# Kernel optimization log

Measured on AMD Instinct MI355X. Metric: run time of the kernel, lower is better.

## Reference

```python
import jax, jax.numpy as jnp
import numpy as np

B, N, D = 8, 1024, 768
H = 12
HD = D // H


def setup_inputs() -> dict:
    key = jax.random.key(0)
    ks = jax.random.split(key, 9)
    s = 1.0 / np.sqrt(D)
    return {
        "x": jax.random.normal(ks[0], (B, N, D), dtype=jnp.float32),
        "Wq": jax.random.normal(ks[1], (D, D), dtype=jnp.float32) * s,
        "bq": jax.random.normal(ks[2], (D,), dtype=jnp.float32) * 0.02,
        "Wk": jax.random.normal(ks[3], (D, D), dtype=jnp.float32) * s,
        "bk": jax.random.normal(ks[4], (D,), dtype=jnp.float32) * 0.02,
        "Wv": jax.random.normal(ks[5], (D, D), dtype=jnp.float32) * s,
        "bv": jax.random.normal(ks[6], (D,), dtype=jnp.float32) * 0.02,
        "Wo": jax.random.normal(ks[7], (D, D), dtype=jnp.float32) * s,
        "bo": jax.random.normal(ks[8], (D,), dtype=jnp.float32) * 0.02,
    }


def _softmax_one(x):
    # quiet softmax: exp(x - max) / (1 + sum exp(x - max))
    x = x - jnp.max(x, axis=-1, keepdims=True)
    ex = jnp.exp(x)
    return ex / (1.0 + jnp.sum(ex, axis=-1, keepdims=True))


def reference(x, Wq, bq, Wk, bk, Wv, bv, Wo, bo):
    q = x @ Wq + bq  # [B,N,D]
    k = x @ Wk + bk
    v = x @ Wv + bv
    # split heads -> [B,H,N,HD]
    qs = q.reshape(B, N, H, HD).transpose(0, 2, 1, 3)
    ks = k.reshape(B, N, H, HD).transpose(0, 2, 1, 3)
    vs = v.reshape(B, N, H, HD).transpose(0, 2, 1, 3)
    scores = jnp.einsum("bhqd,bhkd->bhqk", qs, ks) / np.sqrt(HD)
    attn = _softmax_one(scores)  # quiet_attention=True
    ctx = jnp.einsum("bhqk,bhkd->bhqd", attn, vs)
    ctx = ctx.transpose(0, 2, 1, 3).reshape(B, N, D)
    return ctx @ Wo + bo
```

## Files before the change

### kernel.cpp

```cpp
#include <hip/hip_runtime.h>
#include <cstdint>

#define DEV __device__ __forceinline__

typedef __bf16 bf16x4 __attribute__((ext_vector_type(4)));
typedef __bf16 bf16x8 __attribute__((ext_vector_type(8)));
typedef float  floatx4 __attribute__((ext_vector_type(4)));
typedef float  floatx16 __attribute__((ext_vector_type(16)));
typedef unsigned uint4v __attribute__((ext_vector_type(4)));

constexpr int BB = 8, NSEQ = 1024, DMODEL = 768, NH = 12, HD = 64;
constexpr int MTOK = BB * NSEQ;
constexpr int NQKV = 3 * DMODEL;
constexpr float CS = 0.18033688011112042f;

DEV void async_copy16(void* lds, const void* g) {
    __builtin_amdgcn_global_load_lds(
        (__attribute__((address_space(1))) void*)(const_cast<void*>(g)),
        (__attribute__((address_space(3))) void*)lds,
        16, 0, 0);
}

DEV floatx4 mfma16x32(bf16x8 a, bf16x8 b, floatx4 c) {
    return __builtin_amdgcn_mfma_f32_16x16x32_bf16(a, b, c, 0, 0, 0);
}
DEV floatx16 mfma32x16(bf16x8 a, bf16x8 b, floatx16 c) {
    return __builtin_amdgcn_mfma_f32_32x32x16_bf16(a, b, c, 0, 0, 0);
}
DEV unsigned cvtpk(float a, float b) {
    unsigned r;
    asm("v_cvt_pk_bf16_f32 %0, %1, %2" : "=v"(r) : "v"(a), "v"(b));
    return r;
}
DEV void swap32(unsigned& x, unsigned& y) {
    asm("v_permlane32_swap_b32 %0, %1" : "+v"(x), "+v"(y));
}


__global__ __launch_bounds__(256) void k_prep(const float* __restrict__ x,
                                              __bf16* __restrict__ xb,
                                              const float* __restrict__ Wq,
                                              const float* __restrict__ Wk,
                                              const float* __restrict__ Wv,
                                              const float* __restrict__ Wo,
                                              __bf16* __restrict__ wtqkv,
                                              __bf16* __restrict__ wto,
                                              const float* __restrict__ bq,
                                              const float* __restrict__ bk,
                                              const float* __restrict__ bv,
                                              float* __restrict__ bqkv) {
    __shared__ float tile[32][33];
    int bid = blockIdx.x, t = threadIdx.x;
    if (bid < 6144) {
        int i = (bid * 256 + t) * 4;
        float4 v = *(const float4*)(x + i);
        bf16x4 o;
        o[0] = (__bf16)v.x; o[1] = (__bf16)v.y; o[2] = (__bf16)v.z; o[3] = (__bf16)v.w;
        *(bf16x4*)(xb + i) = o;
    } else if (bid < 8448) {
        int idx = bid - 6144;
        int z = idx / 576, rem = idx % 576;
        int k0 = (rem % 24) * 32, n0 = (rem / 24) * 32;
        const float* W = (z == 0) ? Wq : (z == 1) ? Wk : (z == 2) ? Wv : Wo;
        int tx = t & 31, ty = t >> 5;
#pragma unroll
        for (int p = 0; p < 4; p++)
            tile[ty + 8 * p][tx] = W[(size_t)(k0 + ty + 8 * p) * 768 + n0 + tx];
        __syncthreads();
        __bf16* out = (z < 3) ? (wtqkv + (size_t)z * 768 * 768) : wto;
#pragma unroll
        for (int p = 0; p < 4; p++)
            out[(size_t)(n0 + ty + 8 * p) * 768 + k0 + tx] = (__bf16)tile[tx][ty + 8 * p];
    } else {
        int i = (bid - 8448) * 256 + t;
        if (i < 768) bqkv[i] = bq[i];
        else if (i < 1536) bqkv[i] = bk[i - 768];
        else bqkv[i] = bv[i - 1536];
    }
}

__global__ __launch_bounds__(256) void k_qkv(const __bf16* __restrict__ A,
                                             const __bf16* __restrict__ Bt,
                                             const float* __restrict__ bias,
                                             __bf16* __restrict__ qfb,
                                             __bf16* __restrict__ kfb,
                                             __bf16* __restrict__ vfb) {
    constexpr int SLOT = 8192;
    __shared__ __align__(16) __bf16 lds[3 * SLOT];
    int t = threadIdx.x, lane = t & 63, w = t >> 6;
    int quad = lane >> 4, n16 = lane & 15;
    int wm = w & 1, wn = w >> 1;
    int m0 = blockIdx.x * 128, n0 = blockIdx.y * 128;
    floatx4 acc[4][4] = {};

    auto stage_tile = [&](__bf16* slot, int k0) {
        __bf16* As_ = slot;
        __bf16* Bs_ = slot + 4096;
#pragma unroll
        for (int i = 0; i < 2; i++) {
            int off = t + i * 256;
            int row = off >> 2, pc = off & 3;
            int c = pc ^ ((row >> 1) & 3);
            async_copy16(&As_[row * 32 + pc * 8],
                         &A[(size_t)(m0 + row) * 768 + k0 + c * 8]);
        }
#pragma unroll
        for (int i = 0; i < 2; i++) {
            int off = t + i * 256;
            int row = off >> 2, pc = off & 3;
            int c = pc ^ ((row >> 1) & 3);
            async_copy16(&Bs_[row * 32 + pc * 8],
                         &Bt[(size_t)(n0 + row) * 768 + k0 + c * 8]);
        }
    };

    stage_tile(lds, 0);
    stage_tile(lds + SLOT, 32);
    asm volatile("s_waitcnt vmcnt(4)\n\ts_barrier" ::: "memory");
    __builtin_amdgcn_sched_barrier(0);

#pragma unroll
    for (int kt = 0; kt < 24; kt++) {
        __bf16* As_ = lds + (kt % 3) * SLOT;
        __bf16* Bs_ = As_ + 4096;
        if (kt + 2 < 24) stage_tile(lds + ((kt + 2) % 3) * SLOT, (kt + 2) * 32);

        bf16x8 a[4], bfr[4];
#pragma unroll
        for (int rt = 0; rt < 4; rt++) {
            int row = wm * 64 + rt * 16 + n16;
            a[rt] = *(const bf16x8*)&As_[row * 32 + (quad ^ ((row >> 1) & 3)) * 8];
        }
#pragma unroll
        for (int ct = 0; ct < 4; ct++) {
            int row = wn * 64 + ct * 16 + n16;
            bfr[ct] = *(const bf16x8*)&Bs_[row * 32 + (quad ^ ((row >> 1) & 3)) * 8];
        }
        __builtin_amdgcn_s_setprio(1);
#pragma unroll
        for (int rt = 0; rt < 4; rt++)
#pragma unroll
            for (int ct = 0; ct < 4; ct++)
                acc[rt][ct] = mfma16x32(a[rt], bfr[ct], acc[rt][ct]);
        __builtin_amdgcn_s_setprio(0);

        if (kt < 23) {
            __builtin_amdgcn_sched_barrier(0);
            if (kt < 22) {
                asm volatile("s_waitcnt vmcnt(4)\n\ts_barrier" ::: "memory");
            } else {
                asm volatile("s_waitcnt vmcnt(0)\n\ts_barrier" ::: "memory");
            }
            __builtin_amdgcn_sched_barrier(0);
        }
    }

    if (n0 >= 1536) {
#pragma unroll
        for (int ct = 0; ct < 4; ct++) {
            int col = n0 + wn * 64 + ct * 16 + n16;
            float bs = bias[col];
            int cz = col - 1536;
            int hh = cz >> 6, hd = cz & 63;
            int mg = hd >> 5, l5v = hd & 31;
#pragma unroll
            for (int rt = 0; rt < 4; rt++) {
                int row0 = m0 + wm * 64 + rt * 16 + quad * 4;
                int bb = row0 >> 10, key = row0 & 1023;
                int iw = key >> 7, w_ = (key >> 5) & 3, kc = (key >> 4) & 1;
                int b5v = (key >> 3) & 1, j0 = key & 7;
                bf16x4 pk;
#pragma unroll
                for (int r = 0; r < 4; r++) pk[r] = (__bf16)(acc[rt][ct][r] + bs);
                size_t idx = (((((size_t)(bb * 12 + hh) * 8 + iw) * 4 + w_) * 2 + kc) * 2 + mg) * 512
                             + (size_t)(b5v * 32 + l5v) * 8 + j0;
                *(bf16x4*)&vfb[idx] = pk;
            }
        }
    } else {
        __bf16* dst = (n0 < 768) ? qfb : kfb;
        float mult = (n0 < 768) ? CS : 1.0f;
        bool isQ = (n0 < 768);
        int cofs = isQ ? 0 : 768;
#pragma unroll
        for (int ct = 0; ct < 4; ct++) {
            int col = n0 + wn * 64 + ct * 16 + n16;
            float bs = bias[col];
            int cz = col - cofs;
            int hh = cz >> 6, hd = cz & 63;
            int kfi = hd >> 4, b5v = (hd >> 3) & 1, j = hd & 7;
#pragma unroll
            for (int rt = 0; rt < 4; rt++) {
                int row0 = m0 + wm * 64 + rt * 16 + quad * 4;
                int bb = row0 >> 10, q10 = row0 & 1023;
                size_t idx;
                if (isQ) {
                    int qt = q10 >> 5, l5v = q10 & 31;
                    idx = (((size_t)(bb * 12 + hh) * 32 + qt) * 4 + kfi) * 512
                          + (size_t)(b5v * 32 + l5v) * 8 + j;
                } else {
                    int iw = q10 >> 7, w_ = (q10 >> 5) & 3, l5v = q10 & 31;
                    idx = ((((size_t)(bb * 12 + hh) * 8 + iw) * 4 + w_) * 4 + kfi) * 512
                          + (size_t)(b5v * 32 + l5v) * 8 + j;
                }
#pragma unroll
                for (int r = 0; r < 4; r++)
                    dst[idx + (size_t)r * 8] = (__bf16)((acc[rt][ct][r] + bs) * mult);
            }
        }
    }
}

__global__ __launch_bounds__(256) void k_oproj(const __bf16* __restrict__ A,
                                               const __bf16* __restrict__ Bt,
                                               const float* __restrict__ bias,
                                               float* __restrict__ C) {
    constexpr int SLOT = 6144;
    __shared__ __align__(16) __bf16 lds[3 * SLOT];
    int t = threadIdx.x, lane = t & 63, w = t >> 6;
    int quad = lane >> 4, n16 = lane & 15;
    int wm = w & 1, wn = w >> 1;
    int m0 = blockIdx.x * 128, n0 = blockIdx.y * 64;
    floatx4 acc[4][2] = {};

    auto stage_tile = [&](__bf16* slot, int k0) {
        __bf16* As_ = slot;
        __bf16* Bs_ = slot + 4096;
#pragma unroll
        for (int i = 0; i < 2; i++) {
            int off = t + i * 256;
            int row = off >> 2, pc = off & 3;
            int c = pc ^ ((row >> 1) & 3);
            async_copy16(&As_[row * 32 + pc * 8],
                         &A[(size_t)(m0 + row) * 768 + k0 + c * 8]);
        }
        {
            int off = t;
            int row = off >> 2, pc = off & 3;
            int c = pc ^ ((row >> 1) & 3);
            async_copy16(&Bs_[row * 32 + pc * 8],
                         &Bt[(size_t)(n0 + row) * 768 + k0 + c * 8]);
        }
    };

    stage_tile(lds, 0);
    stage_tile(lds + SLOT, 32);
    asm volatile("s_waitcnt vmcnt(3)\n\ts_barrier" ::: "memory");
    __builtin_amdgcn_sched_barrier(0);

#pragma unroll
    for (int kt = 0; kt < 24; kt++) {
        __bf16* As_ = lds + (kt % 3) * SLOT;
        __bf16* Bs_ = As_ + 4096;
        if (kt + 2 < 24) stage_tile(lds + ((kt + 2) % 3) * SLOT, (kt + 2) * 32);

        bf16x8 a[4], bfr[2];
#pragma unroll
        for (int rt = 0; rt < 4; rt++) {
            int row = wm * 64 + rt * 16 + n16;
            a[rt] = *(const bf16x8*)&As_[row * 32 + (quad ^ ((row >> 1) & 3)) * 8];
        }
#pragma unroll
        for (int ct = 0; ct < 2; ct++) {
            int row = wn * 32 + ct * 16 + n16;
            bfr[ct] = *(const bf16x8*)&Bs_[row * 32 + (quad ^ ((row >> 1) & 3)) * 8];
        }
        __builtin_amdgcn_s_setprio(1);
#pragma unroll
        for (int rt = 0; rt < 4; rt++)
#pragma unroll
            for (int ct = 0; ct < 2; ct++)
                acc[rt][ct] = mfma16x32(a[rt], bfr[ct], acc[rt][ct]);
        __builtin_amdgcn_s_setprio(0);

        if (kt < 23) {
            __builtin_amdgcn_sched_barrier(0);
            if (kt < 22) {
                asm volatile("s_waitcnt vmcnt(3)\n\ts_barrier" ::: "memory");
            } else {
                asm volatile("s_waitcnt vmcnt(0)\n\ts_barrier" ::: "memory");
            }
            __builtin_amdgcn_sched_barrier(0);
        }
    }

#pragma unroll
    for (int ct = 0; ct < 2; ct++) {
        int col = n0 + wn * 32 + ct * 16 + n16;
        float bs = bias[col];
#pragma unroll
        for (int rt = 0; rt < 4; rt++) {
#pragma unroll
            for (int r = 0; r < 4; r++) {
                int row = m0 + wm * 64 + rt * 16 + quad * 4 + r;
                C[(size_t)row * DMODEL + col] = acc[rt][ct][r] + bs;
            }
        }
    }
}

__global__ __launch_bounds__(256) void k_attn(const __bf16* __restrict__ QF,
                                              const __bf16* __restrict__ KF,
                                              const __bf16* __restrict__ VF,
                                              __bf16* __restrict__ ctx) {
    __shared__ __align__(16) unsigned char smem[18432];
    float* buf0 = (float*)smem;
    float* buf1 = (float*)(smem + 8704);
    float* Lsum = (float*)(smem + 17408);
    float* Pmax = (float*)(smem + 17920);

    int t = threadIdx.x, lane = t & 63, w = t >> 6;
    int l5 = lane & 31, b5 = lane >> 5;
    int id = blockIdx.x;
    int bB = id & 7;
    int seq = id >> 3;
    int h = seq % 12;
    int qt = seq / 12;
    int q0 = qt * 32;
    int bh = bB * NH + h;

    bf16x8 qf[4];
    {
        const __bf16* qp = QF + ((size_t)(bh * 32 + qt) * 4) * 512 + lane * 8;
#pragma unroll
        for (int kfi = 0; kfi < 4; kfi++)
            qf[kfi] = *(const bf16x8*)(qp + kfi * 512);
    }
    const __bf16* kp = KF + ((size_t)(bh * 8) * 4 + w) * 2048 + lane * 8;
    const __bf16* vp = VF + ((size_t)(bh * 8) * 4 + w) * 2048 + lane * 8;

    floatx16 acc[2] = {};
    float rs = 0.f, pm = 0.f;

    auto compute = [&](bf16x8 (&kf)[4], bf16x8 (&vf)[4]) {
        floatx16 s = {};
#pragma unroll
        for (int kfi = 0; kfi < 4; kfi++)
            s = mfma32x16(kf[kfi], qf[kfi], s);
        float p[16];
#pragma unroll
        for (int r = 0; r < 16; r++) {
            p[r] = __builtin_amdgcn_exp2f(s[r]);
            rs += p[r];
            pm = fmaxf(pm, p[r]);
        }
        unsigned x0 = cvtpk(p[0], p[1]),   y0 = cvtpk(p[4], p[5]);
        unsigned x1 = cvtpk(p[2], p[3]),   y1 = cvtpk(p[6], p[7]);
        unsigned x2 = cvtpk(p[8], p[9]),   y2 = cvtpk(p[12], p[13]);
        unsigned x3 = cvtpk(p[10], p[11]), y3 = cvtpk(p[14], p[15]);
        swap32(x0, y0); swap32(x1, y1); swap32(x2, y2); swap32(x3, y3);
        uint4v pa = {x0, x1, y0, y1};
        uint4v pbv = {x2, x3, y2, y3};
        bf16x8 P0 = __builtin_bit_cast(bf16x8, pa);
        bf16x8 P1 = __builtin_bit_cast(bf16x8, pbv);
        acc[0] = mfma32x16(vf[0], P0, acc[0]);
        acc[1] = mfma32x16(vf[1], P0, acc[1]);
        acc[0] = mfma32x16(vf[2], P1, acc[0]);
        acc[1] = mfma32x16(vf[3], P1, acc[1]);
    };

    bf16x8 ka[4], kb[4], vv[4];
#pragma unroll
    for (int f = 0; f < 4; f++) ka[f] = *(const bf16x8*)(kp + f * 512);
    kp += 8192;

    for (int i = 0; i < 8; i += 2) {
#pragma unroll
        for (int f = 0; f < 4; f++) kb[f] = *(const bf16x8*)(kp + f * 512);
        kp += 8192;
#pragma unroll
        for (int f = 0; f < 4; f++) vv[f] = *(const bf16x8*)(vp + f * 512);
        vp += 8192;
        compute(ka, vv);
        if (i < 6) {
#pragma unroll
            for (int f = 0; f < 4; f++) ka[f] = *(const bf16x8*)(kp + f * 512);
            kp += 8192;
        }
#pragma unroll
        for (int f = 0; f < 4; f++) vv[f] = *(const bf16x8*)(vp + f * 512);
        vp += 8192;
        compute(kb, vv);
    }

    rs += __shfl_xor(rs, 32);
    pm = fmaxf(pm, __shfl_xor(pm, 32));
    if (lane < 32) {
        Lsum[w * 32 + lane] = rs;
        Pmax[w * 32 + lane] = pm;
    }

    float* mybuf = (w & 1) ? buf1 : buf0;
    if (w < 2) {
#pragma unroll
        for (int mg = 0; mg < 2; mg++)
#pragma unroll
            for (int rq = 0; rq < 4; rq++) {
                floatx4 v = {acc[mg][rq * 4 + 0], acc[mg][rq * 4 + 1],
                             acc[mg][rq * 4 + 2], acc[mg][rq * 4 + 3]};
                *(floatx4*)&mybuf[l5 * 68 + mg * 32 + b5 * 4 + rq * 8] = v;
            }
    }
    __syncthreads();
    if (w >= 2) {
#pragma unroll
        for (int mg = 0; mg < 2; mg++)
#pragma unroll
            for (int rq = 0; rq < 4; rq++) {
                float* p = &mybuf[l5 * 68 + mg * 32 + b5 * 4 + rq * 8];
                floatx4 cur = *(const floatx4*)p;
                floatx4 v = {acc[mg][rq * 4 + 0], acc[mg][rq * 4 + 1],
                             acc[mg][rq * 4 + 2], acc[mg][rq * 4 + 3]};
                *(floatx4*)p = cur + v;
            }
    }
    __syncthreads();

    int qrow = t >> 3;
    int hh = (t & 7) * 8;
    float l = Lsum[qrow] + Lsum[32 + qrow] + Lsum[64 + qrow] + Lsum[96 + qrow];
    float pmx = fmaxf(fmaxf(Pmax[qrow], Pmax[32 + qrow]),
                      fmaxf(Pmax[64 + qrow], Pmax[96 + qrow]));
    float invd = 1.f / (pmx + l);
    floatx4 v0 = *(const floatx4*)&buf0[qrow * 68 + hh];
    floatx4 v1 = *(const floatx4*)&buf0[qrow * 68 + hh + 4];
    floatx4 u0 = *(const floatx4*)&buf1[qrow * 68 + hh];
    floatx4 u1 = *(const floatx4*)&buf1[qrow * 68 + hh + 4];
    bf16x8 o;
#pragma unroll
    for (int j = 0; j < 4; j++) o[j] = (__bf16)((v0[j] + u0[j]) * invd);
#pragma unroll
    for (int j = 0; j < 4; j++) o[j + 4] = (__bf16)((v1[j] + u1[j]) * invd);
    __bf16* dst = ctx + (size_t)(bB * NSEQ + q0 + qrow) * DMODEL + h * 64 + hh;
    *(bf16x8*)dst = o;
}

extern "C" void kernel_launch(void* const* d_in, const int* in_sizes, int n_in,
                              void* d_out, int out_size, void* d_ws, size_t ws_size,
                              hipStream_t stream) {
    (void)in_sizes; (void)n_in; (void)out_size;
    const float* x  = (const float*)d_in[0];
    const float* Wq = (const float*)d_in[1];
    const float* bq = (const float*)d_in[2];
    const float* Wk = (const float*)d_in[3];
    const float* bk = (const float*)d_in[4];
    const float* Wv = (const float*)d_in[5];
    const float* bv = (const float*)d_in[6];
    const float* Wo = (const float*)d_in[7];
    const float* bo = (const float*)d_in[8];
    float* out = (float*)d_out;

    char* ws = (char*)d_ws;
    size_t off = 0;
    auto alloc = [&](size_t bytes) {
        void* p = ws + off;
        off += (bytes + 255) & ~(size_t)255;
        return p;
    };
    __bf16* xb    = (__bf16*)alloc((size_t)MTOK * DMODEL * 2);
    __bf16* wtqkv = (__bf16*)alloc((size_t)NQKV * DMODEL * 2);
    __bf16* wto   = (__bf16*)alloc((size_t)DMODEL * DMODEL * 2);
    float*  bqkv  = (float*)alloc((size_t)NQKV * 4);
    __bf16* qfb   = (__bf16*)alloc((size_t)MTOK * DMODEL * 2);
    __bf16* kfb   = (__bf16*)alloc((size_t)MTOK * DMODEL * 2);
    __bf16* vfb   = (__bf16*)alloc((size_t)MTOK * DMODEL * 2);
    if (off > ws_size) return;
    __bf16* ctx = xb;

    k_prep<<<dim3(8457), dim3(256), 0, stream>>>(x, xb, Wq, Wk, Wv, Wo, wtqkv, wto,
                                                 bq, bk, bv, bqkv);
    k_qkv<<<dim3(64, 18), dim3(256), 0, stream>>>(xb, wtqkv, bqkv, qfb, kfb, vfb);
    k_attn<<<dim3(3072), dim3(256), 0, stream>>>(qfb, kfb, vfb, ctx);
    k_oproj<<<dim3(64, 12), dim3(256), 0, stream>>>(ctx, wto, bo, out);
}
```

Baseline: 189.5 us.

## Replace LDS-staged GEMMs with direct global-to-register double-buffered loads and XCD-aware tiling

The QKV and output-projection GEMMs no longer stage tiles through shared memory with async copies and barriers. Each wave now loads its MFMA fragments straight from global memory into registers, double-buffered across K steps. Block IDs are remapped so neighbouring tiles land on the same XCD for L2 reuse, and the output projection moves to 128-thread blocks computing 64x128 tiles. This removes LDS traffic and barriers, but gives up sharing of loaded data across waves, so global and L2 traffic rises and load latency depends on cache hits.

```diff
diff --git a/kernel.cpp b/kernel.cpp
--- a/kernel.cpp
+++ b/kernel.cpp
@@ -13,13 +13,6 @@
 constexpr int MTOK = BB * NSEQ;
 constexpr int NQKV = 3 * DMODEL;
 constexpr float CS = 0.18033688011112042f;
-
-DEV void async_copy16(void* lds, const void* g) {
-    __builtin_amdgcn_global_load_lds(
-        (__attribute__((address_space(1))) void*)(const_cast<void*>(g)),
-        (__attribute__((address_space(3))) void*)lds,
-        16, 0, 0);
-}
 
 DEV floatx4 mfma16x32(bf16x8 a, bf16x8 b, floatx4 c) {
     return __builtin_amdgcn_mfma_f32_16x16x32_bf16(a, b, c, 0, 0, 0);
@@ -85,74 +78,47 @@
                                              __bf16* __restrict__ qfb,
                                              __bf16* __restrict__ kfb,
                                              __bf16* __restrict__ vfb) {
-    constexpr int SLOT = 8192;
-    __shared__ __align__(16) __bf16 lds[3 * SLOT];
     int t = threadIdx.x, lane = t & 63, w = t >> 6;
     int quad = lane >> 4, n16 = lane & 15;
     int wm = w & 1, wn = w >> 1;
-    int m0 = blockIdx.x * 128, n0 = blockIdx.y * 128;
+    int id = blockIdx.x;
+    int xcd = id & 7, chunk = id >> 3;
+    int bx = (xcd << 3) | (chunk & 7);
+    int by = chunk >> 3;
+    int m0 = bx * 128, n0 = by * 128;
+
+    const __bf16* ap = A + (size_t)(m0 + wm * 64 + n16) * 768 + quad * 8;
+    const __bf16* bp = Bt + (size_t)(n0 + wn * 64 + n16) * 768 + quad * 8;
+
     floatx4 acc[4][4] = {};
-
-    auto stage_tile = [&](__bf16* slot, int k0) {
-        __bf16* As_ = slot;
-        __bf16* Bs_ = slot + 4096;
-#pragma unroll
-        for (int i = 0; i < 2; i++) {
-            int off = t + i * 256;
-            int row = off >> 2, pc = off & 3;
-            int c = pc ^ ((row >> 1) & 3);
-            async_copy16(&As_[row * 32 + pc * 8],
-                         &A[(size_t)(m0 + row) * 768 + k0 + c * 8]);
-        }
-#pragma unroll
-        for (int i = 0; i < 2; i++) {
-            int off = t + i * 256;
-            int row = off >> 2, pc = off & 3;
-            int c = pc ^ ((row >> 1) & 3);
-            async_copy16(&Bs_[row * 32 + pc * 8],
-                         &Bt[(size_t)(n0 + row) * 768 + k0 + c * 8]);
-        }
-    };
-
-    stage_tile(lds, 0);
-    stage_tile(lds + SLOT, 32);
-    asm volatile("s_waitcnt vmcnt(4)\n\ts_barrier" ::: "memory");
-    __builtin_amdgcn_sched_barrier(0);
-
-#pragma unroll
-    for (int kt = 0; kt < 24; kt++) {
-        __bf16* As_ = lds + (kt % 3) * SLOT;
-        __bf16* Bs_ = As_ + 4096;
-        if (kt + 2 < 24) stage_tile(lds + ((kt + 2) % 3) * SLOT, (kt + 2) * 32);
-
-        bf16x8 a[4], bfr[4];
-#pragma unroll
-        for (int rt = 0; rt < 4; rt++) {
-            int row = wm * 64 + rt * 16 + n16;
-            a[rt] = *(const bf16x8*)&As_[row * 32 + (quad ^ ((row >> 1) & 3)) * 8];
-        }
-#pragma unroll
-        for (int ct = 0; ct < 4; ct++) {
-            int row = wn * 64 + ct * 16 + n16;
-            bfr[ct] = *(const bf16x8*)&Bs_[row * 32 + (quad ^ ((row >> 1) & 3)) * 8];
-        }
-        __builtin_amdgcn_s_setprio(1);
+    bf16x8 a0[4], b0[4], a1[4], b1[4];
+
+    auto lda = [&](bf16x8 (&d)[4], int s) {
+#pragma unroll
+        for (int rt = 0; rt < 4; rt++)
+            d[rt] = *(const bf16x8*)(ap + (size_t)rt * 12288 + s * 32);
+    };
+    auto ldb = [&](bf16x8 (&d)[4], int s) {
+#pragma unroll
+        for (int ct = 0; ct < 4; ct++)
+            d[ct] = *(const bf16x8*)(bp + (size_t)ct * 12288 + s * 32);
+    };
+
+    lda(a0, 0); ldb(b0, 0);
+#pragma unroll
+    for (int s = 0; s < 24; s += 2) {
+        lda(a1, s + 1); ldb(b1, s + 1);
 #pragma unroll
         for (int rt = 0; rt < 4; rt++)
 #pragma unroll
             for (int ct = 0; ct < 4; ct++)
-                acc[rt][ct] = mfma16x32(a[rt], bfr[ct], acc[rt][ct]);
-        __builtin_amdgcn_s_setprio(0);
-
-        if (kt < 23) {
-            __builtin_amdgcn_sched_barrier(0);
-            if (kt < 22) {
-                asm volatile("s_waitcnt vmcnt(4)\n\ts_barrier" ::: "memory");
-            } else {
-                asm volatile("s_waitcnt vmcnt(0)\n\ts_barrier" ::: "memory");
-            }
-            __builtin_amdgcn_sched_barrier(0);
-        }
+                acc[rt][ct] = mfma16x32(a0[rt], b0[ct], acc[rt][ct]);
+        if (s < 22) { lda(a0, s + 2); ldb(b0, s + 2); }
+#pragma unroll
+        for (int rt = 0; rt < 4; rt++)
+#pragma unroll
+            for (int ct = 0; ct < 4; ct++)
+                acc[rt][ct] = mfma16x32(a1[rt], b1[ct], acc[rt][ct]);
     }
 
     if (n0 >= 1536) {
@@ -211,88 +177,61 @@
     }
 }
 
-__global__ __launch_bounds__(256) void k_oproj(const __bf16* __restrict__ A,
+__global__ __launch_bounds__(128) void k_oproj(const __bf16* __restrict__ A,
                                                const __bf16* __restrict__ Bt,
                                                const float* __restrict__ bias,
                                                float* __restrict__ C) {
-    constexpr int SLOT = 6144;
-    __shared__ __align__(16) __bf16 lds[3 * SLOT];
-    int t = threadIdx.x, lane = t & 63, w = t >> 6;
+    int t = threadIdx.x, lane = t & 63, wn = t >> 6;
     int quad = lane >> 4, n16 = lane & 15;
-    int wm = w & 1, wn = w >> 1;
-    int m0 = blockIdx.x * 128, n0 = blockIdx.y * 64;
-    floatx4 acc[4][2] = {};
-
-    auto stage_tile = [&](__bf16* slot, int k0) {
-        __bf16* As_ = slot;
-        __bf16* Bs_ = slot + 4096;
-#pragma unroll
-        for (int i = 0; i < 2; i++) {
-            int off = t + i * 256;
-            int row = off >> 2, pc = off & 3;
-            int c = pc ^ ((row >> 1) & 3);
-            async_copy16(&As_[row * 32 + pc * 8],
-                         &A[(size_t)(m0 + row) * 768 + k0 + c * 8]);
-        }
-        {
-            int off = t;
-            int row = off >> 2, pc = off & 3;
-            int c = pc ^ ((row >> 1) & 3);
-            async_copy16(&Bs_[row * 32 + pc * 8],
-                         &Bt[(size_t)(n0 + row) * 768 + k0 + c * 8]);
-        }
-    };
-
-    stage_tile(lds, 0);
-    stage_tile(lds + SLOT, 32);
-    asm volatile("s_waitcnt vmcnt(3)\n\ts_barrier" ::: "memory");
-    __builtin_amdgcn_sched_barrier(0);
-
-#pragma unroll
-    for (int kt = 0; kt < 24; kt++) {
-        __bf16* As_ = lds + (kt % 3) * SLOT;
-        __bf16* Bs_ = As_ + 4096;
-        if (kt + 2 < 24) stage_tile(lds + ((kt + 2) % 3) * SLOT, (kt + 2) * 32);
-
-        bf16x8 a[4], bfr[2];
+    int id = blockIdx.x;
+    int xcd = id & 7, chunk = id >> 3;
+    int bx = (xcd << 4) | (chunk & 15);
+    int by = chunk >> 4;
+    int m0 = bx * 64, n0 = by * 128;
+
+    const __bf16* ap = A + (size_t)(m0 + n16) * 768 + quad * 8;
+    const __bf16* bp = Bt + (size_t)(n0 + wn * 64 + n16) * 768 + quad * 8;
+
+    floatx4 acc[4][4] = {};
+    bf16x8 a0[4], b0[4], a1[4], b1[4];
+
+    auto lda = [&](bf16x8 (&d)[4], int s) {
+#pragma unroll
+        for (int rt = 0; rt < 4; rt++)
+            d[rt] = *(const bf16x8*)(ap + (size_t)rt * 12288 + s * 32);
+    };
+    auto ldb = [&](bf16x8 (&d)[4], int s) {
+#pragma unroll
+        for (int ct = 0; ct < 4; ct++)
+            d[ct] = *(const bf16x8*)(bp + (size_t)ct * 12288 + s * 32);
+    };
+
+    lda(a0, 0); ldb(b0, 0);
+#pragma unroll
+    for (int s = 0; s < 24; s += 2) {
+        lda(a1, s + 1); ldb(b1, s + 1);
+#pragma unroll
+        for (int rt = 0; rt < 4; rt++)
+#pragma unroll
+            for (int ct = 0; ct < 4; ct++)
+                acc[rt][ct] = mfma16x32(a0[rt], b0[ct], acc[rt][ct]);
+        if (s < 22) { lda(a0, s + 2); ldb(b0, s + 2); }
+#pragma unroll
+        for (int rt = 0; rt < 4; rt++)
+#pragma unroll
+            for (int ct = 0; ct < 4; ct++)
+                acc[rt][ct] = mfma16x32(a1[rt], b1[ct], acc[rt][ct]);
+    }
+
+#pragma unroll
+    for (int ct = 0; ct < 4; ct++) {
+        int col = n0 + wn * 64 + ct * 16 + n16;
+        float bs = bias[col];
 #pragma unroll
         for (int rt = 0; rt < 4; rt++) {
-            int row = wm * 64 + rt * 16 + n16;
-            a[rt] = *(const bf16x8*)&As_[row * 32 + (quad ^ ((row >> 1) & 3)) * 8];
-        }
-#pragma unroll
-        for (int ct = 0; ct < 2; ct++) {
-            int row = wn * 32 + ct * 16 + n16;
-            bfr[ct] = *(const bf16x8*)&Bs_[row * 32 + (quad ^ ((row >> 1) & 3)) * 8];
-        }
-        __builtin_amdgcn_s_setprio(1);
-#pragma unroll
-        for (int rt = 0; rt < 4; rt++)
-#pragma unroll
-            for (int ct = 0; ct < 2; ct++)
-                acc[rt][ct] = mfma16x32(a[rt], bfr[ct], acc[rt][ct]);
-        __builtin_amdgcn_s_setprio(0);
-
-        if (kt < 23) {
-            __builtin_amdgcn_sched_barrier(0);
-            if (kt < 22) {
-                asm volatile("s_waitcnt vmcnt(3)\n\ts_barrier" ::: "memory");
-            } else {
-                asm volatile("s_waitcnt vmcnt(0)\n\ts_barrier" ::: "memory");
-            }
-            __builtin_amdgcn_sched_barrier(0);
-        }
-    }
-
-#pragma unroll
-    for (int ct = 0; ct < 2; ct++) {
-        int col = n0 + wn * 32 + ct * 16 + n16;
-        float bs = bias[col];
-#pragma unroll
-        for (int rt = 0; rt < 4; rt++) {
 #pragma unroll
             for (int r = 0; r < 4; r++) {
-                int row = m0 + wm * 64 + rt * 16 + quad * 4 + r;
+                int row = m0 + rt * 16 + quad * 4 + r;
                 C[(size_t)row * DMODEL + col] = acc[rt][ct][r] + bs;
             }
         }
@@ -469,7 +408,7 @@
 
     k_prep<<<dim3(8457), dim3(256), 0, stream>>>(x, xb, Wq, Wk, Wv, Wo, wtqkv, wto,
                                                  bq, bk, bv, bqkv);
-    k_qkv<<<dim3(64, 18), dim3(256), 0, stream>>>(xb, wtqkv, bqkv, qfb, kfb, vfb);
+    k_qkv<<<dim3(1152), dim3(256), 0, stream>>>(xb, wtqkv, bqkv, qfb, kfb, vfb);
     k_attn<<<dim3(3072), dim3(256), 0, stream>>>(qfb, kfb, vfb, ctx);
-    k_oproj<<<dim3(64, 12), dim3(256), 0, stream>>>(ctx, wto, bo, out);
-}
+    k_oproj<<<dim3(768), dim3(128), 0, stream>>>(ctx, wto, bo, out);
+}
```

Measured after the change: 277.3 us. 46.4% more time.

## Switch QKV and out-proj GEMMs to double-buffered BK=64 k-loop

Applied to the files above, without the earlier changes.

Both projection GEMMs now use a two-slot LDS pipeline with a k-step of 64 instead of a three-slot pipeline with a k-step of 32. This halves the number of k iterations and barriers and uses an 8-chunk XOR swizzle on the wider rows. The trade-off is shallower prefetch: only one tile is in flight while computing. Each iteration now has two barriers, and the larger slots use more LDS per block.

```diff
diff --git a/kernel.cpp b/kernel.cpp
--- a/kernel.cpp
+++ b/kernel.cpp
@@ -85,8 +85,8 @@
                                              __bf16* __restrict__ qfb,
                                              __bf16* __restrict__ kfb,
                                              __bf16* __restrict__ vfb) {
-    constexpr int SLOT = 8192;
-    __shared__ __align__(16) __bf16 lds[3 * SLOT];
+    constexpr int SLOT = 16384;
+    __shared__ __align__(16) __bf16 lds[2 * SLOT];
     int t = threadIdx.x, lane = t & 63, w = t >> 6;
     int quad = lane >> 4, n16 = lane & 15;
     int wm = w & 1, wn = w >> 1;
@@ -95,62 +95,66 @@
 
     auto stage_tile = [&](__bf16* slot, int k0) {
         __bf16* As_ = slot;
-        __bf16* Bs_ = slot + 4096;
-#pragma unroll
-        for (int i = 0; i < 2; i++) {
+        __bf16* Bs_ = slot + 8192;
+#pragma unroll
+        for (int i = 0; i < 4; i++) {
             int off = t + i * 256;
-            int row = off >> 2, pc = off & 3;
-            int c = pc ^ ((row >> 1) & 3);
-            async_copy16(&As_[row * 32 + pc * 8],
+            int row = off >> 3, pc = off & 7;
+            int c = pc ^ (row & 7);
+            async_copy16(&As_[row * 64 + pc * 8],
                          &A[(size_t)(m0 + row) * 768 + k0 + c * 8]);
         }
 #pragma unroll
-        for (int i = 0; i < 2; i++) {
+        for (int i = 0; i < 4; i++) {
             int off = t + i * 256;
-            int row = off >> 2, pc = off & 3;
-            int c = pc ^ ((row >> 1) & 3);
-            async_copy16(&Bs_[row * 32 + pc * 8],
+            int row = off >> 3, pc = off & 7;
+            int c = pc ^ (row & 7);
+            async_copy16(&Bs_[row * 64 + pc * 8],
                          &Bt[(size_t)(n0 + row) * 768 + k0 + c * 8]);
         }
     };
 
     stage_tile(lds, 0);
-    stage_tile(lds + SLOT, 32);
-    asm volatile("s_waitcnt vmcnt(4)\n\ts_barrier" ::: "memory");
-    __builtin_amdgcn_sched_barrier(0);
-
-#pragma unroll
-    for (int kt = 0; kt < 24; kt++) {
-        __bf16* As_ = lds + (kt % 3) * SLOT;
-        __bf16* Bs_ = As_ + 4096;
-        if (kt + 2 < 24) stage_tile(lds + ((kt + 2) % 3) * SLOT, (kt + 2) * 32);
-
-        bf16x8 a[4], bfr[4];
-#pragma unroll
-        for (int rt = 0; rt < 4; rt++) {
-            int row = wm * 64 + rt * 16 + n16;
-            a[rt] = *(const bf16x8*)&As_[row * 32 + (quad ^ ((row >> 1) & 3)) * 8];
-        }
-#pragma unroll
-        for (int ct = 0; ct < 4; ct++) {
-            int row = wn * 64 + ct * 16 + n16;
-            bfr[ct] = *(const bf16x8*)&Bs_[row * 32 + (quad ^ ((row >> 1) & 3)) * 8];
-        }
-        __builtin_amdgcn_s_setprio(1);
-#pragma unroll
-        for (int rt = 0; rt < 4; rt++)
-#pragma unroll
-            for (int ct = 0; ct < 4; ct++)
-                acc[rt][ct] = mfma16x32(a[rt], bfr[ct], acc[rt][ct]);
-        __builtin_amdgcn_s_setprio(0);
-
-        if (kt < 23) {
+
+#pragma unroll
+    for (int kt = 0; kt < 12; kt++) {
+        __bf16* As_ = lds + (kt & 1) * SLOT;
+        __bf16* Bs_ = As_ + 8192;
+
+        if (kt + 1 < 12) stage_tile(lds + ((kt + 1) & 1) * SLOT, (kt + 1) * 64);
+        __builtin_amdgcn_sched_barrier(0);
+        if (kt + 1 < 12) {
+            asm volatile("s_waitcnt vmcnt(8)\n\ts_barrier" ::: "memory");
+        } else {
+            asm volatile("s_waitcnt vmcnt(0)\n\ts_barrier" ::: "memory");
+        }
+        __builtin_amdgcn_sched_barrier(0);
+
+#pragma unroll
+        for (int kfi = 0; kfi < 2; kfi++) {
+            bf16x8 a[4], bfr[4];
+#pragma unroll
+            for (int rt = 0; rt < 4; rt++) {
+                int row = wm * 64 + rt * 16 + n16;
+                a[rt] = *(const bf16x8*)&As_[row * 64 + ((quad + 4 * kfi) ^ (row & 7)) * 8];
+            }
+#pragma unroll
+            for (int ct = 0; ct < 4; ct++) {
+                int row = wn * 64 + ct * 16 + n16;
+                bfr[ct] = *(const bf16x8*)&Bs_[row * 64 + ((quad + 4 * kfi) ^ (row & 7)) * 8];
+            }
+            __builtin_amdgcn_s_setprio(1);
+#pragma unroll
+            for (int rt = 0; rt < 4; rt++)
+#pragma unroll
+                for (int ct = 0; ct < 4; ct++)
+                    acc[rt][ct] = mfma16x32(a[rt], bfr[ct], acc[rt][ct]);
+            __builtin_amdgcn_s_setprio(0);
+        }
+
+        if (kt + 1 < 12) {
             __builtin_amdgcn_sched_barrier(0);
-            if (kt < 22) {
-                asm volatile("s_waitcnt vmcnt(4)\n\ts_barrier" ::: "memory");
-            } else {
-                asm volatile("s_waitcnt vmcnt(0)\n\ts_barrier" ::: "memory");
-            }
+            asm volatile("s_barrier" ::: "memory");
             __builtin_amdgcn_sched_barrier(0);
         }
     }
@@ -215,8 +219,8 @@
                                                const __bf16* __restrict__ Bt,
                                                const float* __restrict__ bias,
                                                float* __restrict__ C) {
-    constexpr int SLOT = 6144;
-    __shared__ __align__(16) __bf16 lds[3 * SLOT];
+    constexpr int SLOT = 12288;
+    __shared__ __align__(16) __bf16 lds[2 * SLOT];
     int t = threadIdx.x, lane = t & 63, w = t >> 6;
     int quad = lane >> 4, n16 = lane & 15;
     int wm = w & 1, wn = w >> 1;
@@ -225,61 +229,66 @@
 
     auto stage_tile = [&](__bf16* slot, int k0) {
         __bf16* As_ = slot;
-        __bf16* Bs_ = slot + 4096;
+        __bf16* Bs_ = slot + 8192;
+#pragma unroll
+        for (int i = 0; i < 4; i++) {
+            int off = t + i * 256;
+            int row = off >> 3, pc = off & 7;
+            int c = pc ^ (row & 7);
+            async_copy16(&As_[row * 64 + pc * 8],
+                         &A[(size_t)(m0 + row) * 768 + k0 + c * 8]);
+        }
 #pragma unroll
         for (int i = 0; i < 2; i++) {
             int off = t + i * 256;
-            int row = off >> 2, pc = off & 3;
-            int c = pc ^ ((row >> 1) & 3);
-            async_copy16(&As_[row * 32 + pc * 8],
-                         &A[(size_t)(m0 + row) * 768 + k0 + c * 8]);
-        }
-        {
-            int off = t;
-            int row = off >> 2, pc = off & 3;
-            int c = pc ^ ((row >> 1) & 3);
-            async_copy16(&Bs_[row * 32 + pc * 8],
+            int row = off >> 3, pc = off & 7;
+            int c = pc ^ (row & 7);
+            async_copy16(&Bs_[row * 64 + pc * 8],
                          &Bt[(size_t)(n0 + row) * 768 + k0 + c * 8]);
         }
     };
 
     stage_tile(lds, 0);
-    stage_tile(lds + SLOT, 32);
-    asm volatile("s_waitcnt vmcnt(3)\n\ts_barrier" ::: "memory");
-    __builtin_amdgcn_sched_barrier(0);
-
-#pragma unroll
-    for (int kt = 0; kt < 24; kt++) {
-        __bf16* As_ = lds + (kt % 3) * SLOT;
-        __bf16* Bs_ = As_ + 4096;
-        if (kt + 2 < 24) stage_tile(lds + ((kt + 2) % 3) * SLOT, (kt + 2) * 32);
-
-        bf16x8 a[4], bfr[2];
-#pragma unroll
-        for (int rt = 0; rt < 4; rt++) {
-            int row = wm * 64 + rt * 16 + n16;
-            a[rt] = *(const bf16x8*)&As_[row * 32 + (quad ^ ((row >> 1) & 3)) * 8];
-        }
-#pragma unroll
-        for (int ct = 0; ct < 2; ct++) {
-            int row = wn * 32 + ct * 16 + n16;
-            bfr[ct] = *(const bf16x8*)&Bs_[row * 32 + (quad ^ ((row >> 1) & 3)) * 8];
-        }
-        __builtin_amdgcn_s_setprio(1);
-#pragma unroll
-        for (int rt = 0; rt < 4; rt++)
-#pragma unroll
-            for (int ct = 0; ct < 2; ct++)
-                acc[rt][ct] = mfma16x32(a[rt], bfr[ct], acc[rt][ct]);
-        __builtin_amdgcn_s_setprio(0);
-
-        if (kt < 23) {
+
+#pragma unroll
+    for (int kt = 0; kt < 12; kt++) {
+        __bf16* As_ = lds + (kt & 1) * SLOT;
+        __bf16* Bs_ = As_ + 8192;
+
+        if (kt + 1 < 12) stage_tile(lds + ((kt + 1) & 1) * SLOT, (kt + 1) * 64);
+        __builtin_amdgcn_sched_barrier(0);
+        if (kt + 1 < 12) {
+            asm volatile("s_waitcnt vmcnt(6)\n\ts_barrier" ::: "memory");
+        } else {
+            asm volatile("s_waitcnt vmcnt(0)\n\ts_barrier" ::: "memory");
+        }
+        __builtin_amdgcn_sched_barrier(0);
+
+#pragma unroll
+        for (int kfi = 0; kfi < 2; kfi++) {
+            bf16x8 a[4], bfr[2];
+#pragma unroll
+            for (int rt = 0; rt < 4; rt++) {
+                int row = wm * 64 + rt * 16 + n16;
+                a[rt] = *(const bf16x8*)&As_[row * 64 + ((quad + 4 * kfi) ^ (row & 7)) * 8];
+            }
+#pragma unroll
+            for (int ct = 0; ct < 2; ct++) {
+                int row = wn * 32 + ct * 16 + n16;
+                bfr[ct] = *(const bf16x8*)&Bs_[row * 64 + ((quad + 4 * kfi) ^ (row & 7)) * 8];
+            }
+            __builtin_amdgcn_s_setprio(1);
+#pragma unroll
+            for (int rt = 0; rt < 4; rt++)
+#pragma unroll
+                for (int ct = 0; ct < 2; ct++)
+                    acc[rt][ct] = mfma16x32(a[rt], bfr[ct], acc[rt][ct]);
+            __builtin_amdgcn_s_setprio(0);
+        }
+
+        if (kt + 1 < 12) {
             __builtin_amdgcn_sched_barrier(0);
-            if (kt < 22) {
-                asm volatile("s_waitcnt vmcnt(3)\n\ts_barrier" ::: "memory");
-            } else {
-                asm volatile("s_waitcnt vmcnt(0)\n\ts_barrier" ::: "memory");
-            }
+            asm volatile("s_barrier" ::: "memory");
             __builtin_amdgcn_sched_barrier(0);
         }
     }
```

Result: faster. 183.1 us (-3.4%).
